# Kernel tuning notes

Measured on AMD Instinct MI355X. Metric: run time of the kernel, lower is better.

The kernel has to match this reference:

```python
import jax, jax.numpy as jnp
import numpy as np

B, L, D, H = 2, 2048, 1024, 16
DK = D // H
EPS = 1e-6


def setup_inputs() -> dict:
    key = jax.random.key(0)
    ks = jax.random.split(key, 8)
    s = 0.02
    return {
        "key": jax.random.normal(ks[0], (B, L, D), jnp.float32),
        "value": jax.random.normal(ks[1], (B, L, D), jnp.float32),
        "query": jax.random.normal(ks[2], (B, L, D), jnp.float32),
        "mask": jax.random.randint(ks[3], (B, L, L), 0, 2).astype(bool),
        "W_k": jax.random.normal(ks[4], (D, D), jnp.float32) * s,
        "W_v": jax.random.normal(ks[5], (D, D), jnp.float32) * s,
        "W_q": jax.random.normal(ks[6], (D, D), jnp.float32) * s,
        "ln_g": jnp.ones((D,), jnp.float32),
        "ln_b": jnp.zeros((D,), jnp.float32),
    }


def _mha(key, value, query, mask, W_k, W_v, W_q, ln_g, ln_b):
    b, l, d = key.shape
    # projections (bias=False), split into heads: [b, h, l, dk]
    def proj(x, W):
        return (x @ W).reshape(b, -1, H, DK).transpose(0, 2, 1, 3)
    k_up, v_up, q_up = proj(key, W_k), proj(value, W_v), proj(query, W_q)
    # scores [b, h, q, k]
    scores = jnp.einsum("bhqd,bhkd->bhqk", q_up, k_up) / jnp.sqrt(jnp.asarray(DK, scores_dtype(q_up)))
    scores = jnp.where(mask[:, None, :, :], -1e9, scores)
    attn = jax.nn.softmax(scores, axis=-1)  # dropout = identity (eval mode)
    out = jnp.einsum("bhqk,bhkd->bhqd", attn, v_up)
    out = out.transpose(0, 2, 1, 3).reshape(b, -1, d)
    res = out + query  # res_dropout = identity
    mu = jnp.mean(res, axis=-1, keepdims=True)
    var = jnp.var(res, axis=-1, keepdims=True)
    normed = (res - mu) * jax.lax.rsqrt(var + EPS) * ln_g + ln_b
    return normed, attn.reshape(b * H, attn.shape[2], attn.shape[3])


def scores_dtype(x):
    return x.dtype


def reference(key, value, query, mask, W_k, W_v, W_q, ln_g, ln_b):
    return _mha(key, value, query, mask, W_k, W_v, W_q, ln_g, ln_b)
```

## Files before the change

### kernel.cpp

```cpp
#include <hip/hip_runtime.h>
#include <math.h>

#define BATCH 2
#define SEQ   2048
#define DMODEL 1024
#define NHEAD 16
#define DK    64
#define EPS   1e-6f

typedef unsigned short ushort_t;
typedef __attribute__((ext_vector_type(8))) __bf16 bf16x8;
typedef __attribute__((ext_vector_type(4))) float f32x4;
typedef __attribute__((ext_vector_type(4))) unsigned int uivec4;

union B8U { uivec4 u; bf16x8 v; };

__device__ __forceinline__ ushort_t f2b(float x) {
    union { float f; unsigned int u; } c; c.f = x;
    unsigned int r = (c.u + 0x7fffu + ((c.u >> 16) & 1u)) >> 16;
    return (ushort_t)r;
}
__device__ __forceinline__ float b2f(ushort_t b) {
    union { unsigned int u; float f; } c; c.u = ((unsigned int)b) << 16;
    return c.f;
}
__device__ __forceinline__ bf16x8 ld_frag_lds(const ushort_t* p) {
    B8U t; t.u = *reinterpret_cast<const uivec4*>(p); return t.v;
}
__device__ __forceinline__ bf16x8 ld_frag_glb(const ushort_t* p) {
    B8U t; t.u = *reinterpret_cast<const uivec4*>(p); return t.v;
}
#define MFMA16(a, b, c) __builtin_amdgcn_mfma_f32_16x16x32_bf16((a), (b), (c), 0, 0, 0)

#define AST 40
#define BST 40
__global__ __launch_bounds__(256) void gemm_proj(const float* __restrict__ X,
                                                 const float* __restrict__ W,
                                                 ushort_t* __restrict__ Y) {
    __shared__ __align__(16) ushort_t As[128 * AST];
    __shared__ __align__(16) ushort_t Bt[128 * BST];
    const int t = threadIdx.x;
    const int bm = blockIdx.y * 128;
    const int bn = blockIdx.x * 128;
    const int w = t >> 6, lane = t & 63;
    const int ln16 = lane & 15, quad = lane >> 4;
    const int wr = w >> 1, wc = w & 1;

    f32x4 acc[4][4] = {};

    for (int k0 = 0; k0 < DMODEL; k0 += 32) {
        {
            const int m = t >> 1, half = t & 1;
            const float* src = X + (size_t)(bm + m) * DMODEL + k0 + half * 16;
            ushort_t* dst = &As[m * AST + half * 16];
            #pragma unroll
            for (int i = 0; i < 16; ++i) dst[i] = f2b(src[i]);
        }
        {
            const int kk = t >> 3, n0 = (t & 7) * 16;
            const float* src = W + (size_t)(k0 + kk) * DMODEL + bn + n0;
            #pragma unroll
            for (int i = 0; i < 16; ++i) Bt[(n0 + i) * BST + kk] = f2b(src[i]);
        }
        __syncthreads();
        bf16x8 af[4], bfr[4];
        #pragma unroll
        for (int rt = 0; rt < 4; ++rt)
            af[rt] = ld_frag_lds(&As[(wr * 64 + rt * 16 + ln16) * AST + quad * 8]);
        #pragma unroll
        for (int ct = 0; ct < 4; ++ct)
            bfr[ct] = ld_frag_lds(&Bt[(wc * 64 + ct * 16 + ln16) * BST + quad * 8]);
        #pragma unroll
        for (int rt = 0; rt < 4; ++rt)
            #pragma unroll
            for (int ct = 0; ct < 4; ++ct)
                acc[rt][ct] = MFMA16(af[rt], bfr[ct], acc[rt][ct]);
        __syncthreads();
    }
    #pragma unroll
    for (int rt = 0; rt < 4; ++rt) {
        #pragma unroll
        for (int ct = 0; ct < 4; ++ct) {
            #pragma unroll
            for (int r = 0; r < 4; ++r) {
                int row = bm + wr * 64 + rt * 16 + quad * 4 + r;
                int col = bn + wc * 64 + ct * 16 + ln16;
                Y[(size_t)row * DMODEL + col] = f2b(acc[rt][ct][r]);
            }
        }
    }
}

__global__ __launch_bounds__(256) void transpose_v(const ushort_t* __restrict__ v_up,
                                                   ushort_t* __restrict__ v_t) {
    __shared__ ushort_t tile[64][68];
    const int t = threadIdx.x;
    const int s0 = blockIdx.x * 64;
    const int bh = blockIdx.y;
    const int b = bh >> 4, h = bh & 15;
    {
        const int r = t >> 2, c0 = (t & 3) * 16;
        const ushort_t* src = v_up + ((size_t)b * SEQ + s0 + r) * DMODEL + h * DK + c0;
        #pragma unroll
        for (int i = 0; i < 16; ++i) tile[r][c0 + i] = src[i];
    }
    __syncthreads();
    {
        const int c = t >> 2, r0 = (t & 3) * 16;
        ushort_t* dst = v_t + ((size_t)bh * DK + c) * SEQ + s0 + r0;
        #pragma unroll
        for (int i = 0; i < 16; ++i) dst[i] = tile[r0 + i][c];
    }
}

#define SROW 2056
__global__ __launch_bounds__(512) void attn_fused(const ushort_t* __restrict__ q_up,
                                                  const ushort_t* __restrict__ k_up,
                                                  const ushort_t* __restrict__ v_t,
                                                  const int* __restrict__ mask,
                                                  float* __restrict__ attn,
                                                  float* __restrict__ o_ws) {
    __shared__ __align__(16) ushort_t sS[32 * SROW];
    __shared__ float psum[32][16];
    __shared__ float inv_s[32];

    const int t = threadIdx.x;
    const int w = t >> 6, lane = t & 63;
    const int ln16 = lane & 15, quad = lane >> 4;
    const int q0 = blockIdx.x * 32;
    const int bh = blockIdx.y;
    const int b = bh >> 4, h = bh & 15;

    bf16x8 aq[2][2];
    #pragma unroll
    for (int rt = 0; rt < 2; ++rt)
        #pragma unroll
        for (int ks = 0; ks < 2; ++ks)
            aq[rt][ks] = ld_frag_glb(
                &q_up[((size_t)b * SEQ + q0 + rt * 16 + ln16) * DMODEL + h * DK + ks * 32 + quad * 8]);

    for (int i = 0; i < 16; ++i) {
        const int ct = i * 8 + w;
        const int kt = ct * 16;
        const int col = kt + ln16;
        bf16x8 bk[2];
        #pragma unroll
        for (int ks = 0; ks < 2; ++ks)
            bk[ks] = ld_frag_glb(
                &k_up[((size_t)b * SEQ + kt + ln16) * DMODEL + h * DK + ks * 32 + quad * 8]);
        #pragma unroll
        for (int rt = 0; rt < 2; ++rt) {
            f32x4 c = {0.f, 0.f, 0.f, 0.f};
            c = MFMA16(aq[rt][0], bk[0], c);
            c = MFMA16(aq[rt][1], bk[1], c);
            #pragma unroll
            for (int r = 0; r < 4; ++r) {
                const int row = rt * 16 + quad * 4 + r;
                const int mv = mask[((size_t)b * SEQ + q0 + row) * SEQ + col];
                const float p = mv ? 0.f : __expf(c[r] * 0.125f);
                sS[row * SROW + col] = f2b(p);
            }
        }
    }
    __syncthreads();

    {
        const int row = t >> 4, l16 = t & 15;
        float s = 0.f;
        for (int st = 0; st < 32; ++st) {
            const int col = l16 * 4 + st * 64;
            const ushort_t* p = &sS[row * SROW + col];
            s += b2f(p[0]) + b2f(p[1]) + b2f(p[2]) + b2f(p[3]);
        }
        psum[row][l16] = s;
    }
    __syncthreads();
    if (t < 32) {
        float s = 0.f;
        #pragma unroll
        for (int j = 0; j < 16; ++j) s += psum[t][j];
        inv_s[t] = 1.f / s;
    }
    __syncthreads();

    {
        const int row = t >> 4, l16 = t & 15;
        const float inv = inv_s[row];
        float* arow = attn + ((size_t)bh * SEQ + q0 + row) * SEQ;
        for (int st = 0; st < 32; ++st) {
            const int col = l16 * 4 + st * 64;
            ushort_t* p = &sS[row * SROW + col];
            float4 o;
            float v0 = b2f(p[0]) * inv;
            float v1 = b2f(p[1]) * inv;
            float v2 = b2f(p[2]) * inv;
            float v3 = b2f(p[3]) * inv;
            p[0] = f2b(v0); p[1] = f2b(v1); p[2] = f2b(v2); p[3] = f2b(v3);
            o.x = v0; o.y = v1; o.z = v2; o.w = v3;
            *reinterpret_cast<float4*>(arow + col) = o;
        }
    }
    __syncthreads();

    {
        const int rt = w >> 2, ct = w & 3;
        f32x4 acc = {0.f, 0.f, 0.f, 0.f};
        const ushort_t* arow = &sS[(rt * 16 + ln16) * SROW + quad * 8];
        const ushort_t* vrow = &v_t[((size_t)bh * DK + ct * 16 + ln16) * SEQ + quad * 8];
        #pragma unroll 8
        for (int k0 = 0; k0 < SEQ; k0 += 32) {
            bf16x8 a = ld_frag_lds(arow + k0);
            bf16x8 vb = ld_frag_glb(vrow + k0);
            acc = MFMA16(a, vb, acc);
        }
        #pragma unroll
        for (int r = 0; r < 4; ++r) {
            const int row = q0 + rt * 16 + quad * 4 + r;
            const int col = h * DK + ct * 16 + ln16;
            o_ws[((size_t)b * SEQ + row) * DMODEL + col] = acc[r];
        }
    }
}

__global__ __launch_bounds__(256) void ln_kernel(const float* __restrict__ O,
                                                 const float* __restrict__ Qin,
                                                 const float* __restrict__ g,
                                                 const float* __restrict__ bt,
                                                 float* __restrict__ out) {
    __shared__ float sm[256];
    const int tid = threadIdx.x;
    const size_t base = (size_t)blockIdx.x * DMODEL;
    float v[4];
    float s = 0.f, s2 = 0.f;
    #pragma unroll
    for (int i = 0; i < 4; ++i) {
        int d = tid + i * 256;
        float x = O[base + d] + Qin[base + d];
        v[i] = x;
        s += x;
        s2 += x * x;
    }
    sm[tid] = s; __syncthreads();
    for (int st = 128; st > 0; st >>= 1) {
        if (tid < st) sm[tid] += sm[tid + st];
        __syncthreads();
    }
    s = sm[0]; __syncthreads();
    sm[tid] = s2; __syncthreads();
    for (int st = 128; st > 0; st >>= 1) {
        if (tid < st) sm[tid] += sm[tid + st];
        __syncthreads();
    }
    s2 = sm[0];
    const float mu = s * (1.0f / DMODEL);
    const float var = s2 * (1.0f / DMODEL) - mu * mu;
    const float r = rsqrtf(var + EPS);
    #pragma unroll
    for (int i = 0; i < 4; ++i) {
        int d = tid + i * 256;
        out[base + d] = (v[i] - mu) * r * g[d] + bt[d];
    }
}

extern "C" void kernel_launch(void* const* d_in, const int* in_sizes, int n_in,
                              void* d_out, int out_size, void* d_ws, size_t ws_size,
                              hipStream_t stream) {
    const float* key   = (const float*)d_in[0];
    const float* value = (const float*)d_in[1];
    const float* query = (const float*)d_in[2];
    const int*   mask  = (const int*)  d_in[3];
    const float* W_k   = (const float*)d_in[4];
    const float* W_v   = (const float*)d_in[5];
    const float* W_q   = (const float*)d_in[6];
    const float* ln_g  = (const float*)d_in[7];
    const float* ln_b  = (const float*)d_in[8];

    float* out      = (float*)d_out;
    float* attn_out = out + (size_t)BATCH * SEQ * DMODEL;

    const size_t NPROJ = (size_t)BATCH * SEQ * DMODEL;
    ushort_t* k_up = (ushort_t*)d_ws;
    ushort_t* v_up = k_up + NPROJ;
    ushort_t* q_up = v_up + NPROJ;
    ushort_t* v_t  = q_up + NPROJ;
    float*    o_ws = (float*)(v_t + NPROJ);

    dim3 gproj(DMODEL / 128, (BATCH * SEQ) / 128);
    gemm_proj<<<gproj, 256, 0, stream>>>(key,   W_k, k_up);
    gemm_proj<<<gproj, 256, 0, stream>>>(value, W_v, v_up);
    gemm_proj<<<gproj, 256, 0, stream>>>(query, W_q, q_up);

    dim3 gtr(SEQ / 64, BATCH * NHEAD);
    transpose_v<<<gtr, 256, 0, stream>>>(v_up, v_t);

    dim3 gat(SEQ / 32, BATCH * NHEAD);
    attn_fused<<<gat, 512, 0, stream>>>(q_up, k_up, v_t, mask, attn_out, o_ws);

    ln_kernel<<<BATCH * SEQ, 256, 0, stream>>>(o_ws, query, ln_g, ln_b, out);
}
```

Measured before the change: 1.053 ms.

## Recompute scores in two passes with bit-packed mask and small LDS tile

The attention kernel no longer stages the full 32x2048 probability row block in LDS. A first pass computes only row sums, and a second pass recomputes QK^T, normalizes, streams attn with nontemporal stores and feeds P·V in 256-column chunks. The int mask is packed into bits by a new pre-kernel so both passes read a 32x smaller mask. The three projection GEMMs are merged into one launch. LDS drops sharply, allowing more blocks per CU, at the cost of doing the QK^T matmul and exp twice.

Result: faster. 919.5 us (-12.7%).

```diff
diff --git a/kernel.cpp b/kernel.cpp
--- a/kernel.cpp
+++ b/kernel.cpp
@@ -32,13 +32,40 @@
 }
 #define MFMA16(a, b, c) __builtin_amdgcn_mfma_f32_16x16x32_bf16((a), (b), (c), 0, 0, 0)
 
+__global__ __launch_bounds__(256) void mask_to_bits(const int* __restrict__ mask,
+                                                    unsigned int* __restrict__ bits) {
+    const size_t widx = (size_t)blockIdx.x * 256 + threadIdx.x;
+    const int4* src = reinterpret_cast<const int4*>(mask + widx * 32);
+    unsigned int wv = 0;
+    #pragma unroll
+    for (int i = 0; i < 8; ++i) {
+        int4 v = src[i];
+        wv |= (v.x ? 1u : 0u) << (i * 4 + 0);
+        wv |= (v.y ? 1u : 0u) << (i * 4 + 1);
+        wv |= (v.z ? 1u : 0u) << (i * 4 + 2);
+        wv |= (v.w ? 1u : 0u) << (i * 4 + 3);
+    }
+    bits[widx] = wv;
+}
+
 #define AST 40
 #define BST 40
-__global__ __launch_bounds__(256) void gemm_proj(const float* __restrict__ X,
-                                                 const float* __restrict__ W,
-                                                 ushort_t* __restrict__ Y) {
+__global__ __launch_bounds__(256) void gemm_proj3(const float* __restrict__ X0,
+                                                  const float* __restrict__ X1,
+                                                  const float* __restrict__ X2,
+                                                  const float* __restrict__ W0,
+                                                  const float* __restrict__ W1,
+                                                  const float* __restrict__ W2,
+                                                  ushort_t* __restrict__ Y0,
+                                                  ushort_t* __restrict__ Y1,
+                                                  ushort_t* __restrict__ Y2) {
     __shared__ __align__(16) ushort_t As[128 * AST];
     __shared__ __align__(16) ushort_t Bt[128 * BST];
+    const int z = blockIdx.z;
+    const float* X = (z == 0) ? X0 : (z == 1) ? X1 : X2;
+    const float* W = (z == 0) ? W0 : (z == 1) ? W1 : W2;
+    ushort_t*    Y = (z == 0) ? Y0 : (z == 1) ? Y1 : Y2;
+
     const int t = threadIdx.x;
     const int bm = blockIdx.y * 128;
     const int bn = blockIdx.x * 128;
@@ -113,15 +140,15 @@
     }
 }
 
-#define SROW 2056
-__global__ __launch_bounds__(512) void attn_fused(const ushort_t* __restrict__ q_up,
-                                                  const ushort_t* __restrict__ k_up,
-                                                  const ushort_t* __restrict__ v_t,
-                                                  const int* __restrict__ mask,
-                                                  float* __restrict__ attn,
-                                                  float* __restrict__ o_ws) {
-    __shared__ __align__(16) ushort_t sS[32 * SROW];
-    __shared__ float psum[32][16];
+#define PST 264
+__global__ __launch_bounds__(512, 4) void attn_fused(const ushort_t* __restrict__ q_up,
+                                                     const ushort_t* __restrict__ k_up,
+                                                     const ushort_t* __restrict__ v_t,
+                                                     const unsigned int* __restrict__ mbits,
+                                                     float* __restrict__ attn,
+                                                     float* __restrict__ o_ws) {
+    __shared__ __align__(16) ushort_t Pb[32 * PST];
+    __shared__ float psum[8][32];
     __shared__ float inv_s[32];
 
     const int t = threadIdx.x;
@@ -139,86 +166,107 @@
             aq[rt][ks] = ld_frag_glb(
                 &q_up[((size_t)b * SEQ + q0 + rt * 16 + ln16) * DMODEL + h * DK + ks * 32 + quad * 8]);
 
+    const unsigned int* mrow = mbits + ((size_t)b * SEQ + q0) * (SEQ / 32);
+    const ushort_t* kbase = &k_up[(size_t)b * SEQ * DMODEL + h * DK + quad * 8];
+
+    float rs[2][4] = {};
     for (int i = 0; i < 16; ++i) {
-        const int ct = i * 8 + w;
-        const int kt = ct * 16;
-        const int col = kt + ln16;
-        bf16x8 bk[2];
-        #pragma unroll
-        for (int ks = 0; ks < 2; ++ks)
-            bk[ks] = ld_frag_glb(
-                &k_up[((size_t)b * SEQ + kt + ln16) * DMODEL + h * DK + ks * 32 + quad * 8]);
+        const int kt = (i * 8 + w) * 16;
+        bf16x8 bk0 = ld_frag_glb(kbase + (size_t)(kt + ln16) * DMODEL);
+        bf16x8 bk1 = ld_frag_glb(kbase + (size_t)(kt + ln16) * DMODEL + 32);
+        const int wi = kt >> 5;
+        const int bsh = (kt & 16) + ln16;
         #pragma unroll
         for (int rt = 0; rt < 2; ++rt) {
             f32x4 c = {0.f, 0.f, 0.f, 0.f};
-            c = MFMA16(aq[rt][0], bk[0], c);
-            c = MFMA16(aq[rt][1], bk[1], c);
+            c = MFMA16(aq[rt][0], bk0, c);
+            c = MFMA16(aq[rt][1], bk1, c);
             #pragma unroll
             for (int r = 0; r < 4; ++r) {
                 const int row = rt * 16 + quad * 4 + r;
-                const int mv = mask[((size_t)b * SEQ + q0 + row) * SEQ + col];
-                const float p = mv ? 0.f : __expf(c[r] * 0.125f);
-                sS[row * SROW + col] = f2b(p);
+                const unsigned int mw = mrow[(size_t)row * (SEQ / 32) + wi];
+                const float p = ((mw >> bsh) & 1u) ? 0.f : __expf(c[r] * 0.125f);
+                rs[rt][r] += p;
             }
         }
     }
-    __syncthreads();
-
-    {
-        const int row = t >> 4, l16 = t & 15;
-        float s = 0.f;
-        for (int st = 0; st < 32; ++st) {
-            const int col = l16 * 4 + st * 64;
-            const ushort_t* p = &sS[row * SROW + col];
-            s += b2f(p[0]) + b2f(p[1]) + b2f(p[2]) + b2f(p[3]);
-        }
-        psum[row][l16] = s;
+    #pragma unroll
+    for (int rt = 0; rt < 2; ++rt)
+        #pragma unroll
+        for (int r = 0; r < 4; ++r) {
+            float v = rs[rt][r];
+            v += __shfl_xor(v, 1);
+            v += __shfl_xor(v, 2);
+            v += __shfl_xor(v, 4);
+            v += __shfl_xor(v, 8);
+            rs[rt][r] = v;
+        }
+    if (ln16 == 0) {
+        #pragma unroll
+        for (int rt = 0; rt < 2; ++rt)
+            #pragma unroll
+            for (int r = 0; r < 4; ++r)
+                psum[w][rt * 16 + quad * 4 + r] = rs[rt][r];
     }
     __syncthreads();
     if (t < 32) {
         float s = 0.f;
         #pragma unroll
-        for (int j = 0; j < 16; ++j) s += psum[t][j];
+        for (int j = 0; j < 8; ++j) s += psum[j][t];
         inv_s[t] = 1.f / s;
     }
     __syncthreads();
-
-    {
-        const int row = t >> 4, l16 = t & 15;
-        const float inv = inv_s[row];
-        float* arow = attn + ((size_t)bh * SEQ + q0 + row) * SEQ;
-        for (int st = 0; st < 32; ++st) {
-            const int col = l16 * 4 + st * 64;
-            ushort_t* p = &sS[row * SROW + col];
-            float4 o;
-            float v0 = b2f(p[0]) * inv;
-            float v1 = b2f(p[1]) * inv;
-            float v2 = b2f(p[2]) * inv;
-            float v3 = b2f(p[3]) * inv;
-            p[0] = f2b(v0); p[1] = f2b(v1); p[2] = f2b(v2); p[3] = f2b(v3);
-            o.x = v0; o.y = v1; o.z = v2; o.w = v3;
-            *reinterpret_cast<float4*>(arow + col) = o;
-        }
-    }
-    __syncthreads();
-
-    {
-        const int rt = w >> 2, ct = w & 3;
-        f32x4 acc = {0.f, 0.f, 0.f, 0.f};
-        const ushort_t* arow = &sS[(rt * 16 + ln16) * SROW + quad * 8];
-        const ushort_t* vrow = &v_t[((size_t)bh * DK + ct * 16 + ln16) * SEQ + quad * 8];
-        #pragma unroll 8
-        for (int k0 = 0; k0 < SEQ; k0 += 32) {
-            bf16x8 a = ld_frag_lds(arow + k0);
-            bf16x8 vb = ld_frag_glb(vrow + k0);
+    float invr[2][4];
+    #pragma unroll
+    for (int rt = 0; rt < 2; ++rt)
+        #pragma unroll
+        for (int r = 0; r < 4; ++r)
+            invr[rt][r] = inv_s[rt * 16 + quad * 4 + r];
+
+    const int prt = w >> 2, pct = w & 3;
+    f32x4 acc = {0.f, 0.f, 0.f, 0.f};
+    const ushort_t* vbase = &v_t[((size_t)bh * DK + pct * 16 + ln16) * SEQ + quad * 8];
+    float* abase = attn + ((size_t)bh * SEQ + q0) * SEQ;
+    const ushort_t* prow = &Pb[(prt * 16 + ln16) * PST + quad * 8];
+
+    for (int kb = 0; kb < SEQ; kb += 256) {
+        #pragma unroll
+        for (int tl = 0; tl < 2; ++tl) {
+            const int kt = kb + (w * 2 + tl) * 16;
+            bf16x8 bk0 = ld_frag_glb(kbase + (size_t)(kt + ln16) * DMODEL);
+            bf16x8 bk1 = ld_frag_glb(kbase + (size_t)(kt + ln16) * DMODEL + 32);
+            const int wi = kt >> 5;
+            const int bsh = (kt & 16) + ln16;
+            #pragma unroll
+            for (int rt = 0; rt < 2; ++rt) {
+                f32x4 c = {0.f, 0.f, 0.f, 0.f};
+                c = MFMA16(aq[rt][0], bk0, c);
+                c = MFMA16(aq[rt][1], bk1, c);
+                #pragma unroll
+                for (int r = 0; r < 4; ++r) {
+                    const int row = rt * 16 + quad * 4 + r;
+                    const unsigned int mw = mrow[(size_t)row * (SEQ / 32) + wi];
+                    const float p = ((mw >> bsh) & 1u) ? 0.f : __expf(c[r] * 0.125f);
+                    const float pn = p * invr[rt][r];
+                    __builtin_nontemporal_store(pn, &abase[(size_t)row * SEQ + kt + ln16]);
+                    Pb[row * PST + (kt - kb) + ln16] = f2b(pn);
+                }
+            }
+        }
+        __syncthreads();
+        #pragma unroll
+        for (int k0 = 0; k0 < 256; k0 += 32) {
+            bf16x8 a  = ld_frag_lds(prow + k0);
+            bf16x8 vb = ld_frag_glb(vbase + kb + k0);
             acc = MFMA16(a, vb, acc);
         }
-        #pragma unroll
-        for (int r = 0; r < 4; ++r) {
-            const int row = q0 + rt * 16 + quad * 4 + r;
-            const int col = h * DK + ct * 16 + ln16;
-            o_ws[((size_t)b * SEQ + row) * DMODEL + col] = acc[r];
-        }
+        __syncthreads();
+    }
+    #pragma unroll
+    for (int r = 0; r < 4; ++r) {
+        const int row = q0 + prt * 16 + quad * 4 + r;
+        const int col = h * DK + pct * 16 + ln16;
+        o_ws[((size_t)b * SEQ + row) * DMODEL + col] = acc[r];
     }
 }
 
@@ -284,17 +332,19 @@
     ushort_t* q_up = v_up + NPROJ;
     ushort_t* v_t  = q_up + NPROJ;
     float*    o_ws = (float*)(v_t + NPROJ);
-
-    dim3 gproj(DMODEL / 128, (BATCH * SEQ) / 128);
-    gemm_proj<<<gproj, 256, 0, stream>>>(key,   W_k, k_up);
-    gemm_proj<<<gproj, 256, 0, stream>>>(value, W_v, v_up);
-    gemm_proj<<<gproj, 256, 0, stream>>>(query, W_q, q_up);
+    unsigned int* mbits = (unsigned int*)(o_ws + NPROJ);
+
+    const int nwords = BATCH * SEQ * (SEQ / 32);
+    mask_to_bits<<<nwords / 256, 256, 0, stream>>>(mask, mbits);
+
+    dim3 gproj(DMODEL / 128, (BATCH * SEQ) / 128, 3);
+    gemm_proj3<<<gproj, 256, 0, stream>>>(key, value, query, W_k, W_v, W_q, k_up, v_up, q_up);
 
     dim3 gtr(SEQ / 64, BATCH * NHEAD);
     transpose_v<<<gtr, 256, 0, stream>>>(v_up, v_t);
 
     dim3 gat(SEQ / 32, BATCH * NHEAD);
-    attn_fused<<<gat, 512, 0, stream>>>(q_up, k_up, v_t, mask, attn_out, o_ws);
+    attn_fused<<<gat, 512, 0, stream>>>(q_up, k_up, v_t, mbits, attn_out, o_ws);
 
     ln_kernel<<<BATCH * SEQ, 256, 0, stream>>>(o_ws, query, ln_g, ln_b, out);
 }
```
